# Performance work log

Measured on AMD Instinct MI355X. Metric: run time of the kernel, lower is better.

Reference implementation:

```python
import jax, jax.numpy as jnp
import numpy as np

B, D, Q, E, H, V = 32, 1024, 64, 384, 384, 50000
PAD = 0
EPS = 1e-12


def setup_inputs() -> dict:
    key = jax.random.key(0)
    ks = jax.random.split(key, 13)
    documents = jax.random.randint(ks[0], (B, D), 1, V)
    doc_lens = jax.random.randint(ks[1], (B,), D // 2, D + 1)
    doc_valid = jnp.arange(D)[None, :] < doc_lens[:, None]
    documents = jnp.where(doc_valid, documents, PAD)
    doc_masks = doc_valid.astype(jnp.float32)[:, :, None]
    querys = jax.random.randint(ks[2], (B, Q), 1, V)
    query_lens = jax.random.randint(ks[3], (B,), Q // 2, Q + 1)
    q_valid = jnp.arange(Q)[None, :] < query_lens[:, None]
    querys = jnp.where(q_valid, querys, PAD)
    query_masks = q_valid.astype(jnp.float32)[:, :, None]
    answers = documents[:, :1]  # guaranteed present in each doc
    emb = jax.random.uniform(ks[4], (V + 1, E), jnp.float32, -0.05, 0.05)
    emb = emb.at[PAD].set(0.0)
    gw = lambda k, s: jax.random.normal(k, s, jnp.float32) * 0.05
    w_ih_f = gw(ks[5], (3 * H, E)); w_hh_f = gw(ks[6], (3 * H, H))
    b_ih_f = gw(ks[7], (3 * H,)); b_hh_f = gw(ks[8], (3 * H,))
    w_ih_b = gw(ks[9], (3 * H, E)); w_hh_b = gw(ks[10], (3 * H, H))
    b_ih_b = gw(ks[11], (3 * H,)); b_hh_b = gw(ks[12], (3 * H,))
    return dict(documents=documents, doc_lens=doc_lens, doc_masks=doc_masks,
                querys=querys, query_lens=query_lens, query_masks=query_masks,
                answers=answers, emb=emb,
                w_ih_f=w_ih_f, w_hh_f=w_hh_f, b_ih_f=b_ih_f, b_hh_f=b_hh_f,
                w_ih_b=w_ih_b, w_hh_b=w_hh_b, b_ih_b=b_ih_b, b_hh_b=b_hh_b)


def _gru_dir(x, w_ih, w_hh, b_ih, b_hh):
    # x: [B,T,E] -> outputs [B,T,H]; torch GRU cell math
    Bn = x.shape[0]
    Hn = w_hh.shape[1]
    xp = jnp.einsum('bte,ge->btg', x, w_ih) + b_ih  # precompute input projections [B,T,3H]

    def step(h, g):
        gh = h @ w_hh.T + b_hh
        i_r, i_z, i_n = jnp.split(g, 3, axis=-1)
        h_r, h_z, h_n = jnp.split(gh, 3, axis=-1)
        r = jax.nn.sigmoid(i_r + h_r)
        z = jax.nn.sigmoid(i_z + h_z)
        n = jnp.tanh(i_n + r * h_n)
        hn = (1.0 - z) * n + z * h
        return hn, hn

    h0 = jnp.zeros((Bn, Hn), x.dtype)
    _, out = jax.lax.scan(step, h0, jnp.swapaxes(xp, 0, 1))
    return jnp.swapaxes(out, 0, 1)


def _rev_within_len(x, lens):
    # reverse each sequence only over its valid prefix (emulates packed bwd GRU)
    T = x.shape[1]
    t = jnp.arange(T)
    idx = jnp.where(t[None, :] < lens[:, None], lens[:, None] - 1 - t[None, :], t[None, :])
    return jnp.take_along_axis(x, idx[:, :, None], axis=1)


def _bigru(x, lens, valid, pf, pb):
    out_f = _gru_dir(x, *pf)
    out_b = _rev_within_len(_gru_dir(_rev_within_len(x, lens), *pb), lens)
    out = jnp.concatenate([out_f, out_b], axis=-1)
    return out * valid[:, :, None]  # unpack pads with zeros


def _softmax_mask(x, mask, axis):
    shift = jnp.max(x, axis=axis, keepdims=True)
    e = jnp.exp(x - shift) * mask
    return e / (jnp.sum(e, axis=axis, keepdims=True) + EPS)


def reference(documents, doc_lens, doc_masks, querys, query_lens, query_masks, answers,
              emb, w_ih_f, w_hh_f, b_ih_f, b_hh_f, w_ih_b, w_hh_b, b_ih_b, b_hh_b):
    doc_valid = doc_masks[..., 0]
    q_valid = query_masks[..., 0]
    doc_h = _bigru(emb[documents], doc_lens, doc_valid,
                   (w_ih_f, w_hh_f, b_ih_f, b_hh_f), (w_ih_b, w_hh_b, b_ih_b, b_hh_b))
    q_h = _bigru(emb[querys], query_lens, q_valid,
                 (w_ih_f, w_hh_f, b_ih_f, b_hh_f), (w_ih_b, w_hh_b, b_ih_b, b_hh_b))
    scores = jnp.einsum('bdh,bqh->bdq', doc_h, q_h)          # IndiATT_output
    pair_mask = jnp.einsum('bdo,bqo->bdq', doc_masks, query_masks)
    alpha = _softmax_mask(scores, pair_mask, axis=1)
    beta = _softmax_mask(scores, pair_mask, axis=2)
    beta_aver = jnp.sum(beta, axis=1) / doc_lens[:, None].astype(scores.dtype)  # [B,Q]
    s = jnp.einsum('bdq,bq->bd', alpha, beta_aver)            # AoA_output squeezed
    probs = jnp.sum(s * (documents == answers).astype(s.dtype), axis=1)

    def pick(doc, sv, vv):
        sc = jnp.zeros(V + 1, s.dtype).at[doc].add(sv * vv)   # segment-sum by word id
        cnt = jnp.zeros(V + 1, s.dtype).at[doc].add(vv)
        return jnp.argmax(jnp.where(cnt > 0, sc, -jnp.inf))

    pred_answers = jax.vmap(pick)(documents, s, doc_valid)
    return probs, pred_answers
```

## Files before the change

### kernel.cpp

```cpp
#include <hip/hip_runtime.h>
#include <hip/hip_bf16.h>
#include <stdint.h>

#define EPSV 1e-12f
#define NB 32
#define DD 1024
#define QQ 64
#define EE 384
#define HH 384
#define NW 12

typedef __attribute__((ext_vector_type(4))) float f32x4;
typedef __attribute__((ext_vector_type(8))) __bf16 bf16x8;
typedef __attribute__((ext_vector_type(4))) unsigned short u16x4;
typedef __attribute__((ext_vector_type(4))) int i32x4;
typedef unsigned short u16;

static __device__ __forceinline__ u16 f2bf(float f) {
  union { float f; uint32_t u; } v; v.f = f;
  uint32_t u = v.u;
  return (u16)((u + 0x7fffu + ((u >> 16) & 1u)) >> 16);
}

static __device__ __forceinline__ f32x4 MFMA(bf16x8 a, bf16x8 b, f32x4 c) {
  return __builtin_amdgcn_mfma_f32_16x16x32_bf16(a, b, c, 0, 0, 0);
}

static __device__ __forceinline__ void st_short_sc(u16* p, u16 v) {
  asm volatile("global_store_short %0, %1, off sc1" :: "v"(p), "v"((uint32_t)v) : "memory");
}
static __device__ __forceinline__ void ld_b128_sc(const u16* p, i32x4& d) {
  asm volatile("global_load_dwordx4 %0, %1, off sc1" : "=v"(d) : "v"(p) : "memory");
}
static __device__ __forceinline__ void st_dword_sc(unsigned* p, unsigned v) {
  asm volatile("global_store_dword %0, %1, off sc1" :: "v"(p), "v"(v) : "memory");
}
static __device__ __forceinline__ void ld_tags(const unsigned* p, i32x4& a, i32x4& b, i32x4& c,
                                               i32x4& d, i32x4& e, i32x4& f) {
  asm volatile(
      "global_load_dwordx4 %0, %6, off sc1\n\t"
      "global_load_dwordx4 %1, %6, off offset:16 sc1\n\t"
      "global_load_dwordx4 %2, %6, off offset:32 sc1\n\t"
      "global_load_dwordx4 %3, %6, off offset:48 sc1\n\t"
      "global_load_dwordx4 %4, %6, off offset:64 sc1\n\t"
      "global_load_dwordx4 %5, %6, off offset:80 sc1\n\t"
      "s_waitcnt vmcnt(0)"
      : "=&v"(a), "=&v"(b), "=&v"(c), "=&v"(d), "=&v"(e), "=&v"(f)
      : "v"(p) : "memory");
}

__global__ __launch_bounds__(256) void k_emb(const int* __restrict__ doc, const int* __restrict__ qry,
                                             const float* __restrict__ emb, u16* __restrict__ embx) {
  int i = blockIdx.x * 256 + threadIdx.x;
  int row = i / 96, e4 = i - row * 96;
  int tok = (row < NB * DD) ? doc[row] : qry[row - NB * DD];
  float4 v = ((const float4*)(emb + (size_t)tok * EE))[e4];
  u16x4 o; o.x = f2bf(v.x); o.y = f2bf(v.y); o.z = f2bf(v.z); o.w = f2bf(v.w);
  *(u16x4*)(embx + (size_t)row * EE + e4 * 4) = o;
}

__global__ __launch_bounds__(256) void k_rec(
    const u16* __restrict__ embx,
    const int* __restrict__ doc_lens, const int* __restrict__ q_lens,
    const float* __restrict__ w_ih_f, const float* __restrict__ w_hh_f,
    const float* __restrict__ b_ih_f, const float* __restrict__ b_hh_f,
    const float* __restrict__ w_ih_b, const float* __restrict__ w_hh_b,
    const float* __restrict__ b_ih_b, const float* __restrict__ b_hh_b,
    u16* __restrict__ doc_h, u16* __restrict__ q_h,
    u16* __restrict__ h_bc, unsigned* __restrict__ cnts, unsigned* __restrict__ tags) {
  __shared__ u16 wfrag[73728];
  __shared__ int lensh[32];

  const int grp = blockIdx.x / NW;
  const int wg = blockIdx.x - grp * NW;
  const int corpus = grp >> 1, dir = grp & 1;
  const int T = corpus ? QQ : DD;
  const int* lens = corpus ? q_lens : doc_lens;
  const float* w_ih = dir ? w_ih_b : w_ih_f;
  const float* w_hh = dir ? w_hh_b : w_hh_f;
  const float* b_ih = dir ? b_ih_b : b_ih_f;
  const float* b_hh = dir ? b_hh_b : b_hh_f;
  u16* out = corpus ? q_h : doc_h;
  const u16* ex_base = embx + (corpus ? (size_t)NB * DD * EE : 0);
  u16* hb = h_bc + (size_t)grp * (2 * NB * HH);
  unsigned* cnt = cnts + (size_t)grp * 16;
  const int tid = threadIdx.x;

  if (tid < 32) lensh[tid] = lens[tid];
  for (int idx = tid; idx < 73728; idx += 256) {
    int nt = idx / 12288;
    int rem = idx - nt * 12288;
    int ks = rem >> 9;
    int le = rem & 511;
    int lane_ = le >> 3, i = le & 7;
    int g = nt >> 1, js_ = nt & 1;
    int colw = lane_ & 15, khiw = lane_ >> 4;
    int k = ks * 32 + khiw * 8 + i;
    int rowg = g * 384 + wg * 32 + js_ * 16 + colw;
    float v = (k < 384) ? w_ih[rowg * 384 + k] : w_hh[rowg * 384 + (k - 384)];
    wfrag[idx] = f2bf(v);
  }
  for (int idx = tid; idx < 1024; idx += 256) {
    int b = idx >> 5, jl_ = idx & 31;
    st_short_sc(hb + b * HH + wg * 32 + jl_, (u16)0);
  }
  asm volatile("s_waitcnt vmcnt(0)" ::: "memory");
  __syncthreads();
  if (tid == 0) {
    __hip_atomic_fetch_add(cnt, 1u, __ATOMIC_RELAXED, __HIP_MEMORY_SCOPE_AGENT);
    while (__hip_atomic_load(cnt, __ATOMIC_RELAXED, __HIP_MEMORY_SCOPE_AGENT) < (unsigned)NW)
      __builtin_amdgcn_s_sleep(1);
  }
  __syncthreads();

  const int lane = tid & 63, wv = tid >> 6;
  const int mt = wv >> 1, js = wv & 1;
  const int col = lane & 15, khi = lane >> 4;
  const int jg = wg * 32 + js * 16 + col;
  const float bias_r = b_ih[jg] + b_hh[jg];
  const float bias_z = b_ih[384 + jg] + b_hh[384 + jg];
  const float bias_in = b_ih[768 + jg];
  const float bias_hn = b_hh[768 + jg];
  const int b_x = mt * 16 + col;
  const int len_x = lensh[b_x];
  const int bh0 = mt * 16 + khi * 4;
  int len_h[4];
#pragma unroll
  for (int r = 0; r < 4; ++r) len_h[r] = lensh[bh0 + r];
  const u16* exrow = ex_base + (size_t)b_x * T * EE + khi * 8;
  u16* outp = out + (size_t)dir * HH + jg;
  f32x4 hprev{0.f, 0.f, 0.f, 0.f};

  const unsigned* tagrow = tags + (size_t)grp * 64 + mt * 32;
  unsigned* tagp = tags + (size_t)grp * 64 + mt * 32 + (wg * 2 + js);

  auto trow_of = [&](int s) -> int { return dir ? ((s < len_x) ? (len_x - 1 - s) : s) : s; };
  auto load_ax = [&](bf16x8* ax, int s) {
    const u16* axp = exrow + (size_t)trow_of(s) * EE;
#pragma unroll
    for (int ks = 0; ks < 12; ++ks) ax[ks] = *(const bf16x8*)(axp + ks * 32);
  };
  auto umin2 = [](unsigned a, unsigned b) { return a < b ? a : b; };
  auto pollwait = [&](unsigned need) {
    while (true) {
      i32x4 t0, t1, t2, t3, t4, t5;
      ld_tags(tagrow, t0, t1, t2, t3, t4, t5);
      unsigned mn = 0xffffffffu;
#pragma unroll
      for (int k = 0; k < 4; ++k) {
        mn = umin2(mn, (unsigned)t0[k]); mn = umin2(mn, (unsigned)t1[k]);
        mn = umin2(mn, (unsigned)t2[k]); mn = umin2(mn, (unsigned)t3[k]);
        mn = umin2(mn, (unsigned)t4[k]); mn = umin2(mn, (unsigned)t5[k]);
      }
      if (mn >= need) break;
      __builtin_amdgcn_s_sleep(1);
    }
  };

  bf16x8 axA[12], axB[12];
  load_ax(axA, 0);

  auto step = [&](int s, bf16x8* axc, bf16x8* axn) {
    const int p = s & 1;
    const u16* rbuf = hb + p * (NB * HH);
    u16* wbuf = hb + (p ^ 1) * (NB * HH);
    f32x4 acc_r{0.f, 0.f, 0.f, 0.f};
    f32x4 acc_z = acc_r, acc_nx = acc_r, acc_nh = acc_r;
#pragma unroll
    for (int ks = 0; ks < 12; ++ks) {
      bf16x8 br = *(const bf16x8*)&wfrag[((js) * 24 + ks) * 512 + lane * 8];
      bf16x8 bz = *(const bf16x8*)&wfrag[((2 + js) * 24 + ks) * 512 + lane * 8];
      bf16x8 bn = *(const bf16x8*)&wfrag[((4 + js) * 24 + ks) * 512 + lane * 8];
      acc_r = MFMA(axc[ks], br, acc_r);
      acc_z = MFMA(axc[ks], bz, acc_z);
      acc_nx = MFMA(axc[ks], bn, acc_nx);
    }
    pollwait((unsigned)s);
    i32x4 areg[12];
    const u16* ahp = rbuf + b_x * HH + khi * 8;
#pragma unroll
    for (int ks = 0; ks < 12; ++ks) ld_b128_sc(ahp + ks * 32, areg[ks]);
    asm volatile("s_waitcnt vmcnt(0)" ::: "memory");
    __builtin_amdgcn_sched_barrier(0);
#pragma unroll
    for (int ks = 0; ks < 12; ++ks) {
      bf16x8 af = __builtin_bit_cast(bf16x8, areg[ks]);
      bf16x8 br = *(const bf16x8*)&wfrag[((js) * 24 + 12 + ks) * 512 + lane * 8];
      bf16x8 bz = *(const bf16x8*)&wfrag[((2 + js) * 24 + 12 + ks) * 512 + lane * 8];
      bf16x8 bn = *(const bf16x8*)&wfrag[((4 + js) * 24 + 12 + ks) * 512 + lane * 8];
      acc_r = MFMA(af, br, acc_r);
      acc_z = MFMA(af, bz, acc_z);
      acc_nh = MFMA(af, bn, acc_nh);
    }
    u16 hq[4];
#pragma unroll
    for (int r = 0; r < 4; ++r) {
      const int b = bh0 + r;
      float rg = 1.f / (1.f + __expf(-(acc_r[r] + bias_r)));
      float zg = 1.f / (1.f + __expf(-(acc_z[r] + bias_z)));
      float ng = tanhf(acc_nx[r] + bias_in + rg * (acc_nh[r] + bias_hn));
      float hn = (1.f - zg) * ng + zg * hprev[r];
      hprev[r] = hn;
      hq[r] = f2bf(hn);
      st_short_sc(wbuf + b * HH + jg, hq[r]);
    }
    asm volatile("s_waitcnt vmcnt(0)" ::: "memory");
    if (lane == 0) st_dword_sc(tagp, (unsigned)(s + 1));
    if (s + 1 < T) load_ax(axn, s + 1);
#pragma unroll
    for (int r = 0; r < 4; ++r) {
      const int b = bh0 + r;
      const int len = len_h[r];
      const int tro = dir ? ((s < len) ? (len - 1 - s) : s) : s;
      outp[((size_t)b * T + tro) * (2 * HH)] = hq[r];
    }
  };

  for (int s = 0; s < T; s += 2) {
    step(s, axA, axB);
    step(s + 1, axB, axA);
  }
}

__global__ __launch_bounds__(256) void k_scores(
    const u16* __restrict__ doc_h, const u16* __restrict__ q_h,
    const int* __restrict__ doc_lens, const int* __restrict__ q_lens,
    float* __restrict__ SM, float* __restrict__ rowmax, float* __restrict__ rowsum) {
  const int b = blockIdx.x >> 4, dblk = blockIdx.x & 15;
  const int tid = threadIdx.x, lane = tid & 63, wv = tid >> 6;
  const int col = lane & 15, khi = lane >> 4;
  const int dlen = doc_lens[b], qlen = q_lens[b];
  const u16* dp = doc_h + ((size_t)(b * DD + dblk * 64 + wv * 16 + col)) * (2 * HH) + khi * 8;
  const u16* qp = q_h + (size_t)b * QQ * (2 * HH);
  f32x4 acc[4];
#pragma unroll
  for (int nt = 0; nt < 4; ++nt) acc[nt] = f32x4{0.f, 0.f, 0.f, 0.f};
  for (int ks = 0; ks < 24; ++ks) {
    bf16x8 av = *(const bf16x8*)(dp + ks * 32);
#pragma unroll
    for (int nt = 0; nt < 4; ++nt) {
      bf16x8 bv = *(const bf16x8*)(qp + (size_t)(nt * 16 + col) * (2 * HH) + ks * 32 + khi * 8);
      acc[nt] = MFMA(av, bv, acc[nt]);
    }
  }
  const int d0 = dblk * 64 + wv * 16 + khi * 4;
  float* smb = SM + (size_t)b * DD * QQ;
#pragma unroll
  for (int r = 0; r < 4; ++r) {
    const int d = d0 + r;
    const bool dv = d < dlen;
    float v[4];
#pragma unroll
    for (int nt = 0; nt < 4; ++nt) {
      const int q = nt * 16 + col;
      v[nt] = (dv && q < qlen) ? acc[nt][r] : 0.f;
      smb[(size_t)d * QQ + q] = v[nt];
    }
    float mx = fmaxf(fmaxf(v[0], v[1]), fmaxf(v[2], v[3]));
#pragma unroll
    for (int off = 1; off < 16; off <<= 1) mx = fmaxf(mx, __shfl_xor(mx, off, 64));
    float sm = 0.f;
#pragma unroll
    for (int nt = 0; nt < 4; ++nt) {
      const int q = nt * 16 + col;
      if (dv && q < qlen) sm += __expf(v[nt] - mx);
    }
#pragma unroll
    for (int off = 1; off < 16; off <<= 1) sm += __shfl_xor(sm, off, 64);
    if (col == 0) { rowmax[b * DD + d] = mx; rowsum[b * DD + d] = sm; }
  }
}

__global__ __launch_bounds__(256) void k_cols(
    const float* __restrict__ SM, const float* __restrict__ rowmax, const float* __restrict__ rowsum,
    const int* __restrict__ doc_lens, const int* __restrict__ q_lens,
    float* __restrict__ colmax, float* __restrict__ colsum, float* __restrict__ bav) {
  const int b = blockIdx.x, tid = threadIdx.x;
  const int q = tid & 63, dg = tid >> 6;
  __shared__ float red[4][64];
  __shared__ float cmx[64];
  const float* smb = SM + (size_t)b * DD * QQ;
  float cm = -3.0e38f;
  for (int d = dg; d < DD; d += 4) cm = fmaxf(cm, smb[(size_t)d * QQ + q]);
  red[dg][q] = cm;
  __syncthreads();
  if (tid < 64) cmx[tid] = fmaxf(fmaxf(red[0][tid], red[1][tid]), fmaxf(red[2][tid], red[3][tid]));
  __syncthreads();
  const int dlen = doc_lens[b];
  const bool qv = q < q_lens[b];
  const float cmq = cmx[q];
  float cs = 0.f, ba = 0.f;
  for (int d = dg; d < DD; d += 4) {
    if (qv && d < dlen) {
      float v = smb[(size_t)d * QQ + q];
      cs += __expf(v - cmq);
      ba += __expf(v - rowmax[b * DD + d]) / (rowsum[b * DD + d] + EPSV);
    }
  }
  __syncthreads();
  red[dg][q] = cs;
  __syncthreads();
  float cst = 0.f;
  if (tid < 64) cst = red[0][tid] + red[1][tid] + red[2][tid] + red[3][tid];
  __syncthreads();
  red[dg][q] = ba;
  __syncthreads();
  if (tid < 64) {
    float bat = red[0][tid] + red[1][tid] + red[2][tid] + red[3][tid];
    colmax[b * QQ + tid] = cmx[tid];
    colsum[b * QQ + tid] = cst;
    bav[b * QQ + tid] = bat / (float)dlen;
  }
}

__global__ __launch_bounds__(256) void k_s(
    const float* __restrict__ SM, const float* __restrict__ colmax, const float* __restrict__ colsum,
    const float* __restrict__ bav, const int* __restrict__ doc_lens, const int* __restrict__ q_lens,
    const int* __restrict__ documents, const int* __restrict__ answers,
    float* __restrict__ sc, float* __restrict__ cnt_tok, float* __restrict__ dout) {
  const int b = blockIdx.x >> 2, dblk = blockIdx.x & 3;
  const int tid = threadIdx.x;
  __shared__ float cm[64], cs[64], bv[64];
  __shared__ int qm[64];
  if (tid < 64) {
    cm[tid] = colmax[b * QQ + tid];
    cs[tid] = colsum[b * QQ + tid];
    bv[tid] = bav[b * QQ + tid];
    qm[tid] = (tid < q_lens[b]) ? 1 : 0;
  }
  __syncthreads();
  const int d = dblk * 256 + tid;
  const bool dv = d < doc_lens[b];
  const float* smr = SM + ((size_t)b * DD + d) * QQ;
  float sd = 0.f;
#pragma unroll
  for (int q = 0; q < 64; ++q) {
    float e = (dv && qm[q]) ? __expf(smr[q] - cm[q]) : 0.f;
    sd += e / (cs[q] + EPSV) * bv[q];
  }
  const int tok = documents[b * DD + d];
  if (tok == answers[b]) atomicAdd(&dout[b], sd);
  if (dv) {
    atomicAdd(&sc[(size_t)b * 50001 + tok], sd);
    atomicAdd(&cnt_tok[(size_t)b * 50001 + tok], 1.0f);
  }
}

__global__ __launch_bounds__(256) void k_pred(
    const float* __restrict__ sc, const float* __restrict__ cnt_tok, float* __restrict__ dout) {
  const int b = blockIdx.x, tid = threadIdx.x;
  __shared__ float bvs[256];
  __shared__ int bis[256];
  float bvv = -3.0e38f;
  int bii = 0x7fffffff;
  for (int i = tid; i < 50001; i += 256) {
    if (cnt_tok[(size_t)b * 50001 + i] > 0.f) {
      float v = sc[(size_t)b * 50001 + i];
      if (v > bvv) { bvv = v; bii = i; }
    }
  }
  bvs[tid] = bvv;
  bis[tid] = bii;
  __syncthreads();
  for (int st = 128; st > 0; st >>= 1) {
    if (tid < st) {
      float v2 = bvs[tid + st];
      int i2 = bis[tid + st];
      if (v2 > bvs[tid] || (v2 == bvs[tid] && i2 < bis[tid])) { bvs[tid] = v2; bis[tid] = i2; }
    }
    __syncthreads();
  }
  if (tid == 0) dout[32 + b] = (float)bis[0];
}

extern "C" void kernel_launch(void* const* d_in, const int* in_sizes, int n_in,
                              void* d_out, int out_size, void* d_ws, size_t ws_size,
                              hipStream_t stream) {
  const int* documents = (const int*)d_in[0];
  const int* doc_lens = (const int*)d_in[1];
  const int* querys = (const int*)d_in[3];
  const int* query_lens = (const int*)d_in[4];
  const int* answers = (const int*)d_in[6];
  const float* emb = (const float*)d_in[7];
  const float* w_ih_f = (const float*)d_in[8];
  const float* w_hh_f = (const float*)d_in[9];
  const float* b_ih_f = (const float*)d_in[10];
  const float* b_hh_f = (const float*)d_in[11];
  const float* w_ih_b = (const float*)d_in[12];
  const float* w_hh_b = (const float*)d_in[13];
  const float* b_ih_b = (const float*)d_in[14];
  const float* b_hh_b = (const float*)d_in[15];
  float* dout = (float*)d_out;
  char* ws = (char*)d_ws;

  size_t o = 0;
  auto alloc = [&](size_t bytes) { size_t r = o; o += (bytes + 255) & ~(size_t)255; return r; };
  size_t o_embx = alloc((size_t)34816 * 384 * 2);
  size_t o_doch = alloc((size_t)NB * DD * 768 * 2);
  size_t o_qh   = alloc((size_t)NB * QQ * 768 * 2);
  size_t o_hbc  = alloc((size_t)4 * 2 * NB * HH * 2);
  size_t o_cnt  = alloc((size_t)4 * 16 * 4);
  size_t o_tag  = alloc((size_t)4 * 64 * 4);
  size_t o_sync_end = o;
  size_t o_SM   = alloc((size_t)NB * DD * QQ * 4);
  size_t o_rmax = alloc((size_t)NB * DD * 4);
  size_t o_rsum = alloc((size_t)NB * DD * 4);
  size_t o_cmax = alloc((size_t)NB * QQ * 4);
  size_t o_csum = alloc((size_t)NB * QQ * 4);
  size_t o_bav  = alloc((size_t)NB * QQ * 4);
  size_t o_sc   = alloc((size_t)NB * 50001 * 4);
  size_t o_ctk  = alloc((size_t)NB * 50001 * 4);
  (void)ws_size; (void)in_sizes; (void)n_in; (void)out_size;

  hipMemsetAsync(ws + o_cnt, 0, o_sync_end - o_cnt, stream);
  hipMemsetAsync(ws + o_sc, 0, (o_ctk - o_sc) + (size_t)NB * 50001 * 4, stream);
  hipMemsetAsync(d_out, 0, 64 * sizeof(float), stream);

  k_emb<<<13056, 256, 0, stream>>>(documents, querys, emb, (u16*)(ws + o_embx));
  k_rec<<<48, 256, 0, stream>>>((u16*)(ws + o_embx), doc_lens, query_lens,
                                w_ih_f, w_hh_f, b_ih_f, b_hh_f,
                                w_ih_b, w_hh_b, b_ih_b, b_hh_b,
                                (u16*)(ws + o_doch), (u16*)(ws + o_qh),
                                (u16*)(ws + o_hbc), (unsigned*)(ws + o_cnt), (unsigned*)(ws + o_tag));
  k_scores<<<512, 256, 0, stream>>>((u16*)(ws + o_doch), (u16*)(ws + o_qh), doc_lens, query_lens,
                                    (float*)(ws + o_SM), (float*)(ws + o_rmax), (float*)(ws + o_rsum));
  k_cols<<<32, 256, 0, stream>>>((float*)(ws + o_SM), (float*)(ws + o_rmax), (float*)(ws + o_rsum),
                                 doc_lens, query_lens,
                                 (float*)(ws + o_cmax), (float*)(ws + o_csum), (float*)(ws + o_bav));
  k_s<<<128, 256, 0, stream>>>((float*)(ws + o_SM), (float*)(ws + o_cmax), (float*)(ws + o_csum),
                               (float*)(ws + o_bav), doc_lens, query_lens, documents, answers,
                               (float*)(ws + o_sc), (float*)(ws + o_ctk), dout);
  k_pred<<<32, 256, 0, stream>>>((float*)(ws + o_sc), (float*)(ws + o_ctk), dout);
}
```

Baseline: 5.439 ms.

## Hoist GRU input projection into chunked precompute kernel before recurrence

A new k_xp kernel precomputes the input-side gate projections (W_ih·x plus biases) in fp32 for chunks of 256 timesteps. k_rec now does only the hidden-state MFMAs on each step, and it is relaunched per chunk with the hidden state carried through a global buffer. This takes half of the per-step matrix work off the serial recurrence and halves the LDS weight footprint. In exchange it adds alternating kernel launches that do not overlap each other, plus extra global traffic for the fp32 projections.

```diff
diff --git a/kernel.cpp b/kernel.cpp
--- a/kernel.cpp
+++ b/kernel.cpp
@@ -9,6 +9,7 @@
 #define EE 384
 #define HH 384
 #define NW 12
+#define CH 256
 
 typedef __attribute__((ext_vector_type(4))) float f32x4;
 typedef __attribute__((ext_vector_type(8))) __bf16 bf16x8;
@@ -24,6 +25,15 @@
 
 static __device__ __forceinline__ f32x4 MFMA(bf16x8 a, bf16x8 b, f32x4 c) {
   return __builtin_amdgcn_mfma_f32_16x16x32_bf16(a, b, c, 0, 0, 0);
+}
+
+static __device__ __forceinline__ bf16x8 ldw8(const float* p) {
+  float4 a = *(const float4*)p;
+  float4 b = *(const float4*)(p + 4);
+  union { u16 e[8]; bf16x8 v; } u;
+  u.e[0] = f2bf(a.x); u.e[1] = f2bf(a.y); u.e[2] = f2bf(a.z); u.e[3] = f2bf(a.w);
+  u.e[4] = f2bf(b.x); u.e[5] = f2bf(b.y); u.e[6] = f2bf(b.z); u.e[7] = f2bf(b.w);
+  return u.v;
 }
 
 static __device__ __forceinline__ void st_short_sc(u16* p, u16 v) {
@@ -59,37 +69,97 @@
   *(u16x4*)(embx + (size_t)row * EE + e4 * 4) = o;
 }
 
+__global__ __launch_bounds__(512, 2) void k_xp(
+    const u16* __restrict__ embx, const int* __restrict__ doc_lens, const int* __restrict__ q_lens,
+    const float* __restrict__ w_ih_f, const float* __restrict__ b_ih_f, const float* __restrict__ b_hh_f,
+    const float* __restrict__ w_ih_b, const float* __restrict__ b_ih_b, const float* __restrict__ b_hh_b,
+    float* __restrict__ xpd, float* __restrict__ xpq, int cbase) {
+  __shared__ int lensh[32];
+  const int gx = blockIdx.x;
+  int corpus, d2, jblk, tch;
+  if (gx < 48) { corpus = 0; d2 = gx / 24; int rem = gx % 24; jblk = rem / 4; tch = rem % 4; }
+  else { corpus = 1; int g2 = gx - 48; d2 = g2 / 6; jblk = g2 % 6; tch = 0; }
+  const int T = corpus ? QQ : DD;
+  const int* lens = corpus ? q_lens : doc_lens;
+  const float* w_ih = d2 ? w_ih_b : w_ih_f;
+  const float* b_ih = d2 ? b_ih_b : b_ih_f;
+  const float* b_hh = d2 ? b_hh_b : b_hh_f;
+  const u16* exb = embx + (corpus ? (size_t)NB * DD * EE : 0);
+  float* xpg = corpus ? (xpq + (size_t)d2 * QQ * 36864) : (xpd + (size_t)d2 * CH * 36864);
+  const int tid = threadIdx.x;
+  if (tid < 32) lensh[tid] = lens[tid];
+  __syncthreads();
+  const int lane = tid & 63, wv = tid >> 6;
+  const int wslot = wv >> 1, mt = wv & 1;
+  const int col = lane & 15, khi = lane >> 4;
+  const int jg = jblk * 64 + wslot * 16 + col;
+  const float br = b_ih[jg] + b_hh[jg];
+  const float bz = b_ih[384 + jg] + b_hh[384 + jg];
+  const float bn = b_ih[768 + jg];
+  bf16x8 Wr[12], Wz[12], Wn[12];
+#pragma unroll
+  for (int ks = 0; ks < 12; ++ks) {
+    Wr[ks] = ldw8(w_ih + (size_t)jg * 384 + ks * 32 + khi * 8);
+    Wz[ks] = ldw8(w_ih + (size_t)(384 + jg) * 384 + ks * 32 + khi * 8);
+    Wn[ks] = ldw8(w_ih + (size_t)(768 + jg) * 384 + ks * 32 + khi * 8);
+  }
+  const int b_a = mt * 16 + col;
+  const int lenb = lensh[b_a];
+  const int bh0 = mt * 16 + khi * 4;
+  for (int tt = 0; tt < 64; ++tt) {
+    const int s_lc = tch * 64 + tt;
+    const int s_g = corpus ? s_lc : (cbase + s_lc);
+    const int trow = d2 ? ((s_g < lenb) ? (lenb - 1 - s_g) : s_g) : s_g;
+    const u16* ap = exb + ((size_t)b_a * T + trow) * EE + khi * 8;
+    bf16x8 A[12];
+#pragma unroll
+    for (int ks = 0; ks < 12; ++ks) A[ks] = *(const bf16x8*)(ap + ks * 32);
+    f32x4 ar{0.f, 0.f, 0.f, 0.f}, az = ar, an = ar;
+#pragma unroll
+    for (int ks = 0; ks < 12; ++ks) {
+      ar = MFMA(A[ks], Wr[ks], ar);
+      az = MFMA(A[ks], Wz[ks], az);
+      an = MFMA(A[ks], Wn[ks], an);
+    }
+    float* op = xpg + (size_t)s_lc * 36864 + (size_t)jg * 32 + bh0;
+    f32x4 o0{ar[0] + br, ar[1] + br, ar[2] + br, ar[3] + br};
+    f32x4 o1{az[0] + bz, az[1] + bz, az[2] + bz, az[3] + bz};
+    f32x4 o2{an[0] + bn, an[1] + bn, an[2] + bn, an[3] + bn};
+    *(f32x4*)op = o0;
+    *(f32x4*)(op + 384 * 32) = o1;
+    *(f32x4*)(op + 768 * 32) = o2;
+  }
+}
+
 __global__ __launch_bounds__(256) void k_rec(
-    const u16* __restrict__ embx,
+    const float* __restrict__ xpd, const float* __restrict__ xpq,
     const int* __restrict__ doc_lens, const int* __restrict__ q_lens,
-    const float* __restrict__ w_ih_f, const float* __restrict__ w_hh_f,
-    const float* __restrict__ b_ih_f, const float* __restrict__ b_hh_f,
-    const float* __restrict__ w_ih_b, const float* __restrict__ w_hh_b,
-    const float* __restrict__ b_ih_b, const float* __restrict__ b_hh_b,
+    const float* __restrict__ w_hh_f, const float* __restrict__ b_hh_f,
+    const float* __restrict__ w_hh_b, const float* __restrict__ b_hh_b,
     u16* __restrict__ doc_h, u16* __restrict__ q_h,
-    u16* __restrict__ h_bc, unsigned* __restrict__ cnts, unsigned* __restrict__ tags) {
-  __shared__ u16 wfrag[73728];
+    u16* __restrict__ h_bc, unsigned* __restrict__ cnts, unsigned* __restrict__ tags,
+    float* __restrict__ h_state, int cbase, int first) {
+  __shared__ u16 wfrag[36864];
   __shared__ int lensh[32];
 
   const int grp = blockIdx.x / NW;
   const int wg = blockIdx.x - grp * NW;
   const int corpus = grp >> 1, dir = grp & 1;
   const int T = corpus ? QQ : DD;
+  const int nst = corpus ? QQ : CH;
   const int* lens = corpus ? q_lens : doc_lens;
-  const float* w_ih = dir ? w_ih_b : w_ih_f;
   const float* w_hh = dir ? w_hh_b : w_hh_f;
-  const float* b_ih = dir ? b_ih_b : b_ih_f;
   const float* b_hh = dir ? b_hh_b : b_hh_f;
   u16* out = corpus ? q_h : doc_h;
-  const u16* ex_base = embx + (corpus ? (size_t)NB * DD * EE : 0);
+  const float* xpg = corpus ? (xpq + (size_t)dir * QQ * 36864) : (xpd + (size_t)dir * CH * 36864);
   u16* hb = h_bc + (size_t)grp * (2 * NB * HH);
   unsigned* cnt = cnts + (size_t)grp * 16;
   const int tid = threadIdx.x;
 
   if (tid < 32) lensh[tid] = lens[tid];
-  for (int idx = tid; idx < 73728; idx += 256) {
-    int nt = idx / 12288;
-    int rem = idx - nt * 12288;
+  for (int idx = tid; idx < 36864; idx += 256) {
+    int nt = idx / 6144;
+    int rem = idx - nt * 6144;
     int ks = rem >> 9;
     int le = rem & 511;
     int lane_ = le >> 3, i = le & 7;
@@ -97,49 +167,44 @@
     int colw = lane_ & 15, khiw = lane_ >> 4;
     int k = ks * 32 + khiw * 8 + i;
     int rowg = g * 384 + wg * 32 + js_ * 16 + colw;
-    float v = (k < 384) ? w_ih[rowg * 384 + k] : w_hh[rowg * 384 + (k - 384)];
-    wfrag[idx] = f2bf(v);
-  }
-  for (int idx = tid; idx < 1024; idx += 256) {
-    int b = idx >> 5, jl_ = idx & 31;
-    st_short_sc(hb + b * HH + wg * 32 + jl_, (u16)0);
-  }
-  asm volatile("s_waitcnt vmcnt(0)" ::: "memory");
-  __syncthreads();
-  if (tid == 0) {
-    __hip_atomic_fetch_add(cnt, 1u, __ATOMIC_RELAXED, __HIP_MEMORY_SCOPE_AGENT);
-    while (__hip_atomic_load(cnt, __ATOMIC_RELAXED, __HIP_MEMORY_SCOPE_AGENT) < (unsigned)NW)
-      __builtin_amdgcn_s_sleep(1);
-  }
-  __syncthreads();
+    wfrag[idx] = f2bf(w_hh[(size_t)rowg * 384 + k]);
+  }
+  if (first) {
+    for (int idx = tid; idx < 1024; idx += 256) {
+      int b = idx >> 5, jl_ = idx & 31;
+      st_short_sc(hb + b * HH + wg * 32 + jl_, (u16)0);
+    }
+    asm volatile("s_waitcnt vmcnt(0)" ::: "memory");
+  }
+  __syncthreads();
+  if (first) {
+    if (tid == 0) {
+      __hip_atomic_fetch_add(cnt, 1u, __ATOMIC_RELAXED, __HIP_MEMORY_SCOPE_AGENT);
+      while (__hip_atomic_load(cnt, __ATOMIC_RELAXED, __HIP_MEMORY_SCOPE_AGENT) < (unsigned)NW)
+        __builtin_amdgcn_s_sleep(1);
+    }
+    __syncthreads();
+  }
 
   const int lane = tid & 63, wv = tid >> 6;
   const int mt = wv >> 1, js = wv & 1;
   const int col = lane & 15, khi = lane >> 4;
   const int jg = wg * 32 + js * 16 + col;
-  const float bias_r = b_ih[jg] + b_hh[jg];
-  const float bias_z = b_ih[384 + jg] + b_hh[384 + jg];
-  const float bias_in = b_ih[768 + jg];
   const float bias_hn = b_hh[768 + jg];
   const int b_x = mt * 16 + col;
-  const int len_x = lensh[b_x];
   const int bh0 = mt * 16 + khi * 4;
   int len_h[4];
 #pragma unroll
   for (int r = 0; r < 4; ++r) len_h[r] = lensh[bh0 + r];
-  const u16* exrow = ex_base + (size_t)b_x * T * EE + khi * 8;
   u16* outp = out + (size_t)dir * HH + jg;
-  f32x4 hprev{0.f, 0.f, 0.f, 0.f};
+  f32x4 hprev;
+#pragma unroll
+  for (int r = 0; r < 4; ++r)
+    hprev[r] = first ? 0.f : h_state[(size_t)grp * 12288 + (size_t)jg * 32 + (bh0 + r)];
 
   const unsigned* tagrow = tags + (size_t)grp * 64 + mt * 32;
   unsigned* tagp = tags + (size_t)grp * 64 + mt * 32 + (wg * 2 + js);
 
-  auto trow_of = [&](int s) -> int { return dir ? ((s < len_x) ? (len_x - 1 - s) : s) : s; };
-  auto load_ax = [&](bf16x8* ax, int s) {
-    const u16* axp = exrow + (size_t)trow_of(s) * EE;
-#pragma unroll
-    for (int ks = 0; ks < 12; ++ks) ax[ks] = *(const bf16x8*)(axp + ks * 32);
-  };
   auto umin2 = [](unsigned a, unsigned b) { return a < b ? a : b; };
   auto pollwait = [&](unsigned need) {
     while (true) {
@@ -156,25 +221,21 @@
       __builtin_amdgcn_s_sleep(1);
     }
   };
-
-  bf16x8 axA[12], axB[12];
-  load_ax(axA, 0);
-
-  auto step = [&](int s, bf16x8* axc, bf16x8* axn) {
+  auto load_xp = [&](f32x4* x, int sl) {
+    const float* xs = xpg + (size_t)sl * 36864;
+#pragma unroll
+    for (int g = 0; g < 3; ++g)
+      x[g] = *(const f32x4*)(xs + ((size_t)(g * 384 + jg)) * 32 + bh0);
+  };
+
+  f32x4 xpA[3], xpB[3];
+  load_xp(xpA, 0);
+
+  auto step = [&](int sl, f32x4* xc, f32x4* xn) {
+    const int s = cbase + sl;
     const int p = s & 1;
     const u16* rbuf = hb + p * (NB * HH);
     u16* wbuf = hb + (p ^ 1) * (NB * HH);
-    f32x4 acc_r{0.f, 0.f, 0.f, 0.f};
-    f32x4 acc_z = acc_r, acc_nx = acc_r, acc_nh = acc_r;
-#pragma unroll
-    for (int ks = 0; ks < 12; ++ks) {
-      bf16x8 br = *(const bf16x8*)&wfrag[((js) * 24 + ks) * 512 + lane * 8];
-      bf16x8 bz = *(const bf16x8*)&wfrag[((2 + js) * 24 + ks) * 512 + lane * 8];
-      bf16x8 bn = *(const bf16x8*)&wfrag[((4 + js) * 24 + ks) * 512 + lane * 8];
-      acc_r = MFMA(axc[ks], br, acc_r);
-      acc_z = MFMA(axc[ks], bz, acc_z);
-      acc_nx = MFMA(axc[ks], bn, acc_nx);
-    }
     pollwait((unsigned)s);
     i32x4 areg[12];
     const u16* ahp = rbuf + b_x * HH + khi * 8;
@@ -182,12 +243,14 @@
     for (int ks = 0; ks < 12; ++ks) ld_b128_sc(ahp + ks * 32, areg[ks]);
     asm volatile("s_waitcnt vmcnt(0)" ::: "memory");
     __builtin_amdgcn_sched_barrier(0);
+    f32x4 acc_r{0.f, 0.f, 0.f, 0.f};
+    f32x4 acc_z = acc_r, acc_nh = acc_r;
 #pragma unroll
     for (int ks = 0; ks < 12; ++ks) {
       bf16x8 af = __builtin_bit_cast(bf16x8, areg[ks]);
-      bf16x8 br = *(const bf16x8*)&wfrag[((js) * 24 + 12 + ks) * 512 + lane * 8];
-      bf16x8 bz = *(const bf16x8*)&wfrag[((2 + js) * 24 + 12 + ks) * 512 + lane * 8];
-      bf16x8 bn = *(const bf16x8*)&wfrag[((4 + js) * 24 + 12 + ks) * 512 + lane * 8];
+      bf16x8 br = *(const bf16x8*)&wfrag[((js) * 12 + ks) * 512 + lane * 8];
+      bf16x8 bz = *(const bf16x8*)&wfrag[((2 + js) * 12 + ks) * 512 + lane * 8];
+      bf16x8 bn = *(const bf16x8*)&wfrag[((4 + js) * 12 + ks) * 512 + lane * 8];
       acc_r = MFMA(af, br, acc_r);
       acc_z = MFMA(af, bz, acc_z);
       acc_nh = MFMA(af, bn, acc_nh);
@@ -196,9 +259,9 @@
 #pragma unroll
     for (int r = 0; r < 4; ++r) {
       const int b = bh0 + r;
-      float rg = 1.f / (1.f + __expf(-(acc_r[r] + bias_r)));
-      float zg = 1.f / (1.f + __expf(-(acc_z[r] + bias_z)));
-      float ng = tanhf(acc_nx[r] + bias_in + rg * (acc_nh[r] + bias_hn));
+      float rg = 1.f / (1.f + __expf(-(acc_r[r] + xc[0][r])));
+      float zg = 1.f / (1.f + __expf(-(acc_z[r] + xc[1][r])));
+      float ng = tanhf(xc[2][r] + rg * (acc_nh[r] + bias_hn));
       float hn = (1.f - zg) * ng + zg * hprev[r];
       hprev[r] = hn;
       hq[r] = f2bf(hn);
@@ -206,7 +269,7 @@
     }
     asm volatile("s_waitcnt vmcnt(0)" ::: "memory");
     if (lane == 0) st_dword_sc(tagp, (unsigned)(s + 1));
-    if (s + 1 < T) load_ax(axn, s + 1);
+    load_xp(xn, (sl + 1 < nst) ? (sl + 1) : sl);
 #pragma unroll
     for (int r = 0; r < 4; ++r) {
       const int b = bh0 + r;
@@ -216,10 +279,13 @@
     }
   };
 
-  for (int s = 0; s < T; s += 2) {
-    step(s, axA, axB);
-    step(s + 1, axB, axA);
-  }
+  for (int sl = 0; sl < nst; sl += 2) {
+    step(sl, xpA, xpB);
+    step(sl + 1, xpB, xpA);
+  }
+#pragma unroll
+  for (int r = 0; r < 4; ++r)
+    h_state[(size_t)grp * 12288 + (size_t)jg * 32 + (bh0 + r)] = hprev[r];
 }
 
 __global__ __launch_bounds__(256) void k_scores(
@@ -396,9 +462,12 @@
   size_t o = 0;
   auto alloc = [&](size_t bytes) { size_t r = o; o += (bytes + 255) & ~(size_t)255; return r; };
   size_t o_embx = alloc((size_t)34816 * 384 * 2);
+  size_t o_xpd  = alloc((size_t)2 * CH * 36864 * 4);
+  size_t o_xpq  = alloc((size_t)2 * QQ * 36864 * 4);
   size_t o_doch = alloc((size_t)NB * DD * 768 * 2);
   size_t o_qh   = alloc((size_t)NB * QQ * 768 * 2);
   size_t o_hbc  = alloc((size_t)4 * 2 * NB * HH * 2);
+  size_t o_hst  = alloc((size_t)4 * HH * NB * 4);
   size_t o_cnt  = alloc((size_t)4 * 16 * 4);
   size_t o_tag  = alloc((size_t)4 * 64 * 4);
   size_t o_sync_end = o;
@@ -417,11 +486,19 @@
   hipMemsetAsync(d_out, 0, 64 * sizeof(float), stream);
 
   k_emb<<<13056, 256, 0, stream>>>(documents, querys, emb, (u16*)(ws + o_embx));
-  k_rec<<<48, 256, 0, stream>>>((u16*)(ws + o_embx), doc_lens, query_lens,
-                                w_ih_f, w_hh_f, b_ih_f, b_hh_f,
-                                w_ih_b, w_hh_b, b_ih_b, b_hh_b,
-                                (u16*)(ws + o_doch), (u16*)(ws + o_qh),
-                                (u16*)(ws + o_hbc), (unsigned*)(ws + o_cnt), (unsigned*)(ws + o_tag));
+  for (int c = 0; c < 4; ++c) {
+    const int cbase = c * CH;
+    k_xp<<<c == 0 ? 60 : 48, 512, 0, stream>>>(
+        (u16*)(ws + o_embx), doc_lens, query_lens,
+        w_ih_f, b_ih_f, b_hh_f, w_ih_b, b_ih_b, b_hh_b,
+        (float*)(ws + o_xpd), (float*)(ws + o_xpq), cbase);
+    k_rec<<<c == 0 ? 48 : 24, 256, 0, stream>>>(
+        (float*)(ws + o_xpd), (float*)(ws + o_xpq), doc_lens, query_lens,
+        w_hh_f, b_hh_f, w_hh_b, b_hh_b,
+        (u16*)(ws + o_doch), (u16*)(ws + o_qh),
+        (u16*)(ws + o_hbc), (unsigned*)(ws + o_cnt), (unsigned*)(ws + o_tag),
+        (float*)(ws + o_hst), cbase, c == 0 ? 1 : 0);
+  }
   k_scores<<<512, 256, 0, stream>>>((u16*)(ws + o_doch), (u16*)(ws + o_qh), doc_lens, query_lens,
                                     (float*)(ws + o_SM), (float*)(ws + o_rmax), (float*)(ws + o_rsum));
   k_cols<<<32, 256, 0, stream>>>((float*)(ws + o_SM), (float*)(ws + o_rmax), (float*)(ws + o_rsum),
```

After: 5.779 ms. +6.3%, slower.
